# Kernel optimization log

Hardware: AMD Instinct MI355X
Metric: run time of the kernel (lower is better)

## Reference

```python
import jax, jax.numpy as jnp
import numpy as np

N = 50000      # nodes
E = 600000     # edges
F_IN = 128     # num_node_features
H = 128        # hidden_channels
C = 10         # num_classes
G = 128        # graphs in batch


def setup_inputs() -> dict:
    key = jax.random.key(0)
    ks = jax.random.split(key, 12)
    x = jax.random.normal(ks[0], (N, F_IN), dtype=jnp.float32)
    edge_index = jax.random.randint(ks[1], (2, E), 0, N, dtype=jnp.int64)
    batch = jnp.sort(jax.random.randint(ks[2], (N,), 0, G, dtype=jnp.int64))
    s = 0.05
    return {
        "x": x,
        "W1": jax.random.normal(ks[3], (F_IN, H), jnp.float32) * s,
        "b1": jnp.zeros((H,), jnp.float32),
        "W2": jax.random.normal(ks[4], (H, H), jnp.float32) * s,
        "b2": jnp.zeros((H,), jnp.float32),
        "W3": jax.random.normal(ks[5], (H, H), jnp.float32) * s,
        "b3": jnp.zeros((H,), jnp.float32),
        "Wl": jax.random.normal(ks[6], (H, C), jnp.float32) * s,
        "bl": jnp.zeros((C,), jnp.float32),
        "edge_index": edge_index,
        "batch": batch,
    }


def _gcn_conv(h, W, b, src, dst, norm, n):
    # h: [N, din] -> linear (no bias), gather, scale, scatter-add, + bias
    h = h @ W                                  # [N, dout]
    msg = norm[:, None] * h[src]               # [E+N, dout]
    out = jax.ops.segment_sum(msg, dst, num_segments=n)
    return out + b


def reference(x, W1, b1, W2, b2, W3, b3, Wl, bl, edge_index, batch):
    n = x.shape[0]
    # add self-loops (PyG GCNConv default) and symmetric normalization
    loop = jnp.arange(n, dtype=edge_index.dtype)
    src = jnp.concatenate([edge_index[0], loop])   # [E+N]
    dst = jnp.concatenate([edge_index[1], loop])   # [E+N]
    deg = jax.ops.segment_sum(jnp.ones_like(dst, dtype=x.dtype), dst, num_segments=n)
    dinv = jnp.where(deg > 0, jax.lax.rsqrt(deg), 0.0)
    norm = dinv[src] * dinv[dst]                   # [E+N]

    h = jax.nn.relu(_gcn_conv(x, W1, b1, src, dst, norm, n))
    h = jax.nn.relu(_gcn_conv(h, W2, b2, src, dst, norm, n))
    h = jax.nn.relu(_gcn_conv(h, W3, b3, src, dst, norm, n))

    # global mean pool over graph ids
    sums = jax.ops.segment_sum(h, batch, num_segments=G)           # [G, H]
    cnts = jax.ops.segment_sum(jnp.ones((n,), h.dtype), batch, num_segments=G)
    pooled = sums / jnp.maximum(cnts, 1.0)[:, None]

    # dropout is identity at inference; final linear classifier
    return pooled @ Wl + bl                                        # [G, C]
```

## Files before the change

kernel.cpp:

```cpp
#include <hip/hip_runtime.h>

#define HID 128
#define CLS 10
#define RCAP 64

typedef short short8 __attribute__((ext_vector_type(8)));
typedef float f32x4 __attribute__((ext_vector_type(4)));

__device__ __forceinline__ unsigned short f2bf(float f) {
  union { float f; unsigned u; } v; v.f = f;
  unsigned u = v.u;
  return (unsigned short)((u + 0x7FFFu + ((u >> 16) & 1u)) >> 16);
}
__device__ __forceinline__ float bf_lo(unsigned p) { return __uint_as_float(p << 16); }
__device__ __forceinline__ float bf_hi(unsigned p) { return __uint_as_float(p & 0xFFFF0000u); }


__global__ __launch_bounds__(256) void zero_init(int* __restrict__ degi, int n,
                                                 float* __restrict__ pooled, int gh,
                                                 unsigned short* __restrict__ TzA,
                                                 unsigned short* __restrict__ TzB) {
  int i = blockIdx.x * 256 + threadIdx.x;
  if (i < n) degi[i] = 0;
  if (i < gh) pooled[i] = 0.f;
  if (blockIdx.x == 0 && threadIdx.x < 16) {
    uint4 z; z.x = z.y = z.z = z.w = 0u;
    *(uint4*)&TzA[threadIdx.x * 8] = z;
    *(uint4*)&TzB[threadIdx.x * 8] = z;
  }
}

__global__ __launch_bounds__(256) void degree_fill_wt(const int* __restrict__ src,
                                                      const int* __restrict__ dst,
                                                      int* __restrict__ degi,
                                                      int* __restrict__ col_src, int E, int nbE,
                                                      const float* __restrict__ W1,
                                                      const float* __restrict__ W2,
                                                      const float* __restrict__ W3,
                                                      unsigned short* __restrict__ Wt) {
  int b = blockIdx.x;
  if (b < nbE) {
    int e = b * 256 + threadIdx.x;
    if (e >= E) return;
    int d = dst[e];
    int slot = atomicAdd(&degi[d], 1);
    if (slot < RCAP) col_src[(size_t)d * RCAP + slot] = src[e];
    return;
  }
  int wb = b - nbE;
  int mat = wb >> 4;
  int part = wb & 15;
  const float* W = (mat == 0) ? W1 : (mat == 1) ? W2 : W3;
  unsigned short* o = Wt + (size_t)mat * HID * HID;
  int base = part * (HID * HID / 16);
  for (int r = 0; r < HID * HID / 16; r += 256) {
    int idx = base + r + threadIdx.x;
    int k = idx >> 7, nn = idx & 127;
    o[nn * HID + k] = f2bf(W[idx]);
  }
}


#define WTP 136

__global__ __launch_bounds__(256) void gemm_mfma(const float* __restrict__ Aptr,
                                                 const unsigned short* __restrict__ Wt,
                                                 const int* __restrict__ degi,
                                                 unsigned short* __restrict__ Tb,
                                                 int* __restrict__ pad_col,
                                                 int nrows) {
  __shared__ unsigned short sW[HID][WTP];
  int tid = threadIdx.x;
  int wave = tid >> 6, lane = tid & 63;
  int m_lo = lane & 15, quad = lane >> 4;
  int row0 = blockIdx.x * 128;
  int rbase = row0 + wave * 32;

  uint4 araw[2][4];
#pragma unroll
  for (int tr = 0; tr < 2; ++tr) {
    int grow = rbase + tr * 16 + m_lo;
    int gr = (grow < nrows) ? grow : (nrows - 1);
    const float* Arow = Aptr + (size_t)gr * HID;
#pragma unroll
    for (int kb = 0; kb < 4; ++kb) {
      float4 f0 = *(const float4*)&Arow[kb * 32 + quad * 8];
      float4 f1 = *(const float4*)&Arow[kb * 32 + quad * 8 + 4];
      uint4 u;
      u.x = (unsigned)f2bf(f0.x) | ((unsigned)f2bf(f0.y) << 16);
      u.y = (unsigned)f2bf(f0.z) | ((unsigned)f2bf(f0.w) << 16);
      u.z = (unsigned)f2bf(f1.x) | ((unsigned)f2bf(f1.y) << 16);
      u.w = (unsigned)f2bf(f1.z) | ((unsigned)f2bf(f1.w) << 16);
      araw[tr][kb] = u;
    }
  }

  const uint4* Wt4 = (const uint4*)Wt;
#pragma unroll
  for (int i = 0; i < 8; ++i) {
    int idx = i * 256 + tid;
    *(uint4*)&sW[idx >> 4][(idx & 15) * 8] = Wt4[idx];
  }
  __syncthreads();

  f32x4 acc[2][8];
#pragma unroll
  for (int tr = 0; tr < 2; ++tr)
#pragma unroll
    for (int tc = 0; tc < 8; ++tc) acc[tr][tc] = (f32x4)(0.f);

#pragma unroll
  for (int kb = 0; kb < 4; ++kb) {
    short8 b[8];
#pragma unroll
    for (int tc = 0; tc < 8; ++tc) {
      union { uint4 u; short8 s; } cv;
      cv.u = *(const uint4*)&sW[tc * 16 + m_lo][kb * 32 + quad * 8];
      b[tc] = cv.s;
    }
#pragma unroll
    for (int tr = 0; tr < 2; ++tr) {
      union { uint4 u; short8 s; } av;
      av.u = araw[tr][kb];
#pragma unroll
      for (int tc = 0; tc < 8; ++tc)
        acc[tr][tc] = __builtin_amdgcn_mfma_f32_16x16x32_bf16(av.s, b[tc], acc[tr][tc], 0, 0, 0);
    }
  }

#pragma unroll
  for (int tr = 0; tr < 2; ++tr) {
#pragma unroll
    for (int r = 0; r < 4; ++r) {
      int grow = rbase + tr * 16 + quad * 4 + r;
      if (grow < nrows) {
        int dgv = degi[grow];
        float s = rsqrtf((float)dgv + 1.0f);
        unsigned short* orow = &Tb[(size_t)grow * HID];
#pragma unroll
        for (int tc = 0; tc < 8; ++tc)
          orow[tc * 16 + m_lo] = f2bf(s * acc[tr][tc][r]);
        if (m_lo == 0) {
          int d = dgv < RCAP ? dgv : RCAP;
          int dp = (d + 3) & ~3;
          for (int sl = d; sl < dp; ++sl)
            pad_col[(size_t)grow * RCAP + sl] = nrows;
        }
      }
    }
  }
}


__device__ __forceinline__ void agg_node(const unsigned* __restrict__ Tb2,
                                         const int* __restrict__ degi,
                                         const int* __restrict__ col_src,
                                         const float* __restrict__ bias,
                                         int node, int l4, float a[8]) {
  uint4 sv = *(const uint4*)&Tb2[(size_t)node * 64 + l4 * 4];
  a[0] = bf_lo(sv.x); a[1] = bf_hi(sv.x); a[2] = bf_lo(sv.y); a[3] = bf_hi(sv.y);
  a[4] = bf_lo(sv.z); a[5] = bf_hi(sv.z); a[6] = bf_lo(sv.w); a[7] = bf_hi(sv.w);
  int deg = degi[node];
  int dc = deg < RCAP ? deg : RCAP;
  int dp = (dc + 3) & ~3;
  const int* row = &col_src[(size_t)node * RCAP];
  int j = 0;
  for (; j + 8 <= dp; j += 8) {
    int idx[8];
#pragma unroll
    for (int u = 0; u < 8; ++u) idx[u] = row[j + u];
    uint4 v[8];
#pragma unroll
    for (int u = 0; u < 8; ++u) v[u] = *(const uint4*)&Tb2[(size_t)idx[u] * 64 + l4 * 4];
#pragma unroll
    for (int u = 0; u < 8; ++u) {
      a[0] += bf_lo(v[u].x); a[1] += bf_hi(v[u].x);
      a[2] += bf_lo(v[u].y); a[3] += bf_hi(v[u].y);
      a[4] += bf_lo(v[u].z); a[5] += bf_hi(v[u].z);
      a[6] += bf_lo(v[u].w); a[7] += bf_hi(v[u].w);
    }
  }
  if (j < dp) {
    int idx[4];
#pragma unroll
    for (int u = 0; u < 4; ++u) idx[u] = row[j + u];
    uint4 v[4];
#pragma unroll
    for (int u = 0; u < 4; ++u) v[u] = *(const uint4*)&Tb2[(size_t)idx[u] * 64 + l4 * 4];
#pragma unroll
    for (int u = 0; u < 4; ++u) {
      a[0] += bf_lo(v[u].x); a[1] += bf_hi(v[u].x);
      a[2] += bf_lo(v[u].y); a[3] += bf_hi(v[u].y);
      a[4] += bf_lo(v[u].z); a[5] += bf_hi(v[u].z);
      a[6] += bf_lo(v[u].w); a[7] += bf_hi(v[u].w);
    }
  }
  float di = rsqrtf((float)deg + 1.0f);
  float4 bs0 = *(const float4*)&bias[l4 * 8];
  float4 bs1 = *(const float4*)&bias[l4 * 8 + 4];
  a[0] = fmaxf(di * a[0] + bs0.x, 0.f);
  a[1] = fmaxf(di * a[1] + bs0.y, 0.f);
  a[2] = fmaxf(di * a[2] + bs0.z, 0.f);
  a[3] = fmaxf(di * a[3] + bs0.w, 0.f);
  a[4] = fmaxf(di * a[4] + bs1.x, 0.f);
  a[5] = fmaxf(di * a[5] + bs1.y, 0.f);
  a[6] = fmaxf(di * a[6] + bs1.z, 0.f);
  a[7] = fmaxf(di * a[7] + bs1.w, 0.f);
}


__global__ __launch_bounds__(256, 4) void fused_agg_gemm(const unsigned* __restrict__ Tb_in,
                                                         const int* __restrict__ degi,
                                                         const int* __restrict__ col_src,
                                                         const float* __restrict__ bias,
                                                         const unsigned short* __restrict__ Wt,
                                                         unsigned short* __restrict__ Tb_out,
                                                         int n) {
  __shared__ unsigned short sW[HID][WTP];
  __shared__ unsigned short sH[16][WTP];
  int tid = threadIdx.x;

  const uint4* Wt4 = (const uint4*)Wt;
#pragma unroll
  for (int i = 0; i < 8; ++i) {
    int idx = i * 256 + tid;
    *(uint4*)&sW[idx >> 4][(idx & 15) * 8] = Wt4[idx];
  }

  int nl = tid >> 4, l4 = tid & 15;
  int node = blockIdx.x * 16 + nl;
  int nodec = node < n ? node : (n - 1);
  float a[8];
  agg_node(Tb_in, degi, col_src, bias, nodec, l4, a);
  uint4 o;
  o.x = (unsigned)f2bf(a[0]) | ((unsigned)f2bf(a[1]) << 16);
  o.y = (unsigned)f2bf(a[2]) | ((unsigned)f2bf(a[3]) << 16);
  o.z = (unsigned)f2bf(a[4]) | ((unsigned)f2bf(a[5]) << 16);
  o.w = (unsigned)f2bf(a[6]) | ((unsigned)f2bf(a[7]) << 16);
  *(uint4*)&sH[nl][l4 * 8] = o;
  __syncthreads();

  int wid = tid >> 6, lane = tid & 63;
  int m_lo = lane & 15, quad = lane >> 4;
  f32x4 acc[2];
  acc[0] = (f32x4)(0.f); acc[1] = (f32x4)(0.f);
#pragma unroll
  for (int kb = 0; kb < 4; ++kb) {
    union { uint4 u; short8 s; } av;
    av.u = *(const uint4*)&sH[m_lo][kb * 32 + quad * 8];
#pragma unroll
    for (int t = 0; t < 2; ++t) {
      int tc = wid * 2 + t;
      union { uint4 u; short8 s; } bv;
      bv.u = *(const uint4*)&sW[tc * 16 + m_lo][kb * 32 + quad * 8];
      acc[t] = __builtin_amdgcn_mfma_f32_16x16x32_bf16(av.s, bv.s, acc[t], 0, 0, 0);
    }
  }
#pragma unroll
  for (int r = 0; r < 4; ++r) {
    int grow = blockIdx.x * 16 + quad * 4 + r;
    if (grow < n) {
      float s = rsqrtf((float)degi[grow] + 1.0f);
      unsigned short* orow = &Tb_out[(size_t)grow * HID];
#pragma unroll
      for (int t = 0; t < 2; ++t) {
        int tc = wid * 2 + t;
        orow[tc * 16 + m_lo] = f2bf(s * acc[t][r]);
      }
    }
  }
}

#define SPP 132

__global__ __launch_bounds__(256) void aggregate_pool(const unsigned* __restrict__ Tb2,
                                                      const int* __restrict__ degi,
                                                      const int* __restrict__ col_src,
                                                      const float* __restrict__ bias,
                                                      const int* __restrict__ batch,
                                                      float* __restrict__ pooled, int n) {
  __shared__ float sP[16][SPP];
  int tid = threadIdx.x;
  int wave = tid >> 6, lane = tid & 63;
  int sub = lane >> 4;
  int l4 = lane & 15;
  int base = blockIdx.x * 16;
  int nl = wave * 4 + sub;
  int node = base + nl;
  bool active = (node < n);

  float a[8] = {0.f, 0.f, 0.f, 0.f, 0.f, 0.f, 0.f, 0.f};
  if (active) agg_node(Tb2, degi, col_src, bias, node, l4, a);
  *(float4*)&sP[nl][l4 * 8] = make_float4(a[0], a[1], a[2], a[3]);
  *(float4*)&sP[nl][l4 * 8 + 4] = make_float4(a[4], a[5], a[6], a[7]);
  __syncthreads();

  if (tid < HID) {
    int g = -1;
    float acc = 0.f;
    for (int i = 0; i < 16; ++i) {
      int nd = base + i;
      if (nd >= n) break;
      int bi = batch[nd];
      if (bi != g) {
        if (g >= 0) atomicAdd(&pooled[g * HID + tid], acc);
        acc = 0.f;
        g = bi;
      }
      acc += sP[i][tid];
    }
    if (g >= 0) atomicAdd(&pooled[g * HID + tid], acc);
  }
}

__global__ __launch_bounds__(128) void classify_k(const float* __restrict__ pooled,
                                                  const int* __restrict__ batch,
                                                  const float* __restrict__ Wl,
                                                  const float* __restrict__ bl,
                                                  float* __restrict__ out, int n) {
  int g = blockIdx.x;
  int t = threadIdx.x;
  int lo = 0, hi = n;
  while (lo < hi) { int mid = (lo + hi) >> 1; if (batch[mid] < g) lo = mid + 1; else hi = mid; }
  int s = lo;
  hi = n;
  while (lo < hi) { int mid = (lo + hi) >> 1; if (batch[mid] < g + 1) lo = mid + 1; else hi = mid; }
  float c = fmaxf((float)(lo - s), 1.0f);
  __shared__ float p[HID];
  p[t] = pooled[g * HID + t] / c;
  __syncthreads();
  if (t < CLS) {
    float o = bl[t];
    for (int j = 0; j < HID; ++j) o += p[j] * Wl[j * CLS + t];
    out[g * CLS + t] = o;
  }
}


extern "C" void kernel_launch(void* const* d_in, const int* in_sizes, int n_in,
                              void* d_out, int out_size, void* d_ws, size_t ws_size,
                              hipStream_t stream) {
  const float* x  = (const float*)d_in[0];
  const float* W1 = (const float*)d_in[1];
  const float* b1 = (const float*)d_in[2];
  const float* W2 = (const float*)d_in[3];
  const float* b2 = (const float*)d_in[4];
  const float* W3 = (const float*)d_in[5];
  const float* b3 = (const float*)d_in[6];
  const float* Wl = (const float*)d_in[7];
  const float* bl = (const float*)d_in[8];
  const int* edge_index = (const int*)d_in[9];
  const int* batch = (const int*)d_in[10];

  const int N = in_sizes[10];
  const int E = in_sizes[9] / 2;
  const int G = out_size / CLS;
  const int* src = edge_index;
  const int* dst = edge_index + E;

  uintptr_t p = (uintptr_t)d_ws;
  auto take = [&](size_t bytes) -> void* {
    void* r = (void*)p;
    p += (bytes + 255) & ~(size_t)255;
    return r;
  };
  int*      degi      = (int*)take((size_t)N * 4);
  int*      col_src   = (int*)take((size_t)N * RCAP * 4);
  unsigned short* WtA = (unsigned short*)take((size_t)3 * HID * HID * 2);
  unsigned short* bufTa = (unsigned short*)take((size_t)(N + 1) * HID * 2);
  unsigned short* bufTb = (unsigned short*)take((size_t)(N + 1) * HID * 2);
  float*    pooled    = (float*)take((size_t)G * HID * 4);

  int nbN = (N + 255) / 256;
  int nbE = (E + 255) / 256;

  zero_init<<<nbN, 256, 0, stream>>>(degi, N, pooled, G * HID,
                                     bufTa + (size_t)N * HID, bufTb + (size_t)N * HID);
  degree_fill_wt<<<nbE + 48, 256, 0, stream>>>(src, dst, degi, col_src, E, nbE,
                                               W1, W2, W3, WtA);

  int gemmBlocks = (N + 127) / 128;
  int aggBlocks = (N + 15) / 16;

  gemm_mfma<<<gemmBlocks, 256, 0, stream>>>(x, WtA, degi, bufTa, col_src, N);
  fused_agg_gemm<<<aggBlocks, 256, 0, stream>>>((unsigned*)bufTa, degi, col_src, b1,
                                                WtA + (size_t)HID * HID, bufTb, N);
  fused_agg_gemm<<<aggBlocks, 256, 0, stream>>>((unsigned*)bufTb, degi, col_src, b2,
                                                WtA + (size_t)2 * HID * HID, bufTa, N);
  aggregate_pool<<<aggBlocks, 256, 0, stream>>>((unsigned*)bufTa, degi, col_src, b3,
                                                batch, pooled, N);
  classify_k<<<G, 128, 0, stream>>>(pooled, batch, Wl, bl, (float*)d_out, N);
}
```

Measured before the change: 226.0 us.

## Split feature matrix into column slices and aggregate one slice per launch

Stores the bf16 node-feature buffers as four 32-column slices, each of 64 bytes per node, instead of 128-column rows. Each aggregation pass then gathers from a single slice across several launches, so the gathered working set is smaller and more likely to stay in cache. Four lanes cooperate on each neighbor list and combine their partial sums with shuffles. The fused aggregate+GEMM kernel now aggregates only the last slice and reads the other three from an intermediate buffer. This adds extra launches, an extra buffer round trip and repeated index-list reads.

```diff
diff --git a/kernel.cpp b/kernel.cpp
--- a/kernel.cpp
+++ b/kernel.cpp
@@ -6,6 +6,7 @@
 
 typedef short short8 __attribute__((ext_vector_type(8)));
 typedef float f32x4 __attribute__((ext_vector_type(4)));
+
 
 __device__ __forceinline__ unsigned short f2bf(float f) {
   union { float f; unsigned u; } v; v.f = f;
@@ -18,15 +19,18 @@
 
 __global__ __launch_bounds__(256) void zero_init(int* __restrict__ degi, int n,
                                                  float* __restrict__ pooled, int gh,
-                                                 unsigned short* __restrict__ TzA,
-                                                 unsigned short* __restrict__ TzB) {
+                                                 unsigned short* __restrict__ Ta,
+                                                 unsigned short* __restrict__ Tb) {
   int i = blockIdx.x * 256 + threadIdx.x;
   if (i < n) degi[i] = 0;
   if (i < gh) pooled[i] = 0.f;
-  if (blockIdx.x == 0 && threadIdx.x < 16) {
+  if (blockIdx.x == 0 && threadIdx.x < 32) {
+    int buf = threadIdx.x >> 4;
+    int s = (threadIdx.x >> 2) & 3;
+    int c = threadIdx.x & 3;
+    unsigned short* T = buf ? Tb : Ta;
     uint4 z; z.x = z.y = z.z = z.w = 0u;
-    *(uint4*)&TzA[threadIdx.x * 8] = z;
-    *(uint4*)&TzB[threadIdx.x * 8] = z;
+    *(uint4*)&T[((size_t)s * (n + 1) + n) * 32 + c * 8] = z;
   }
 }
 
@@ -136,10 +140,10 @@
       if (grow < nrows) {
         int dgv = degi[grow];
         float s = rsqrtf((float)dgv + 1.0f);
-        unsigned short* orow = &Tb[(size_t)grow * HID];
 #pragma unroll
         for (int tc = 0; tc < 8; ++tc)
-          orow[tc * 16 + m_lo] = f2bf(s * acc[tr][tc][r]);
+          Tb[((size_t)(tc >> 1) * (nrows + 1) + grow) * 32 + (tc & 1) * 16 + m_lo] =
+              f2bf(s * acc[tr][tc][r]);
         if (m_lo == 0) {
           int d = dgv < RCAP ? dgv : RCAP;
           int dp = (d + 3) & ~3;
@@ -152,69 +156,84 @@
 }
 
 
-__device__ __forceinline__ void agg_node(const unsigned* __restrict__ Tb2,
-                                         const int* __restrict__ degi,
-                                         const int* __restrict__ col_src,
-                                         const float* __restrict__ bias,
-                                         int node, int l4, float a[8]) {
-  uint4 sv = *(const uint4*)&Tb2[(size_t)node * 64 + l4 * 4];
-  a[0] = bf_lo(sv.x); a[1] = bf_hi(sv.x); a[2] = bf_lo(sv.y); a[3] = bf_hi(sv.y);
-  a[4] = bf_lo(sv.z); a[5] = bf_hi(sv.z); a[6] = bf_lo(sv.w); a[7] = bf_hi(sv.w);
-  int deg = degi[node];
-  int dc = deg < RCAP ? deg : RCAP;
-  int dp = (dc + 3) & ~3;
-  const int* row = &col_src[(size_t)node * RCAP];
-  int j = 0;
-  for (; j + 8 <= dp; j += 8) {
-    int idx[8];
-#pragma unroll
-    for (int u = 0; u < 8; ++u) idx[u] = row[j + u];
-    uint4 v[8];
-#pragma unroll
-    for (int u = 0; u < 8; ++u) v[u] = *(const uint4*)&Tb2[(size_t)idx[u] * 64 + l4 * 4];
-#pragma unroll
-    for (int u = 0; u < 8; ++u) {
-      a[0] += bf_lo(v[u].x); a[1] += bf_hi(v[u].x);
-      a[2] += bf_lo(v[u].y); a[3] += bf_hi(v[u].y);
-      a[4] += bf_lo(v[u].z); a[5] += bf_hi(v[u].z);
-      a[6] += bf_lo(v[u].w); a[7] += bf_hi(v[u].w);
-    }
+__device__ __forceinline__ void slice_gather(const unsigned short* __restrict__ Tslice,
+                                             const int* __restrict__ row,
+                                             int node, int dp, int q, int sub, float a[8]) {
+  if (q == 0) {
+    uint4 sv = *(const uint4*)&Tslice[(size_t)node * 32 + sub * 8];
+    a[0] = bf_lo(sv.x); a[1] = bf_hi(sv.x); a[2] = bf_lo(sv.y); a[3] = bf_hi(sv.y);
+    a[4] = bf_lo(sv.z); a[5] = bf_hi(sv.z); a[6] = bf_lo(sv.w); a[7] = bf_hi(sv.w);
+  } else {
+#pragma unroll
+    for (int k = 0; k < 8; ++k) a[k] = 0.f;
+  }
+  int j = q;
+  for (; j + 4 < dp; j += 8) {
+    int i0 = row[j], i1 = row[j + 4];
+    uint4 v0 = *(const uint4*)&Tslice[(size_t)i0 * 32 + sub * 8];
+    uint4 v1 = *(const uint4*)&Tslice[(size_t)i1 * 32 + sub * 8];
+    a[0] += bf_lo(v0.x); a[1] += bf_hi(v0.x); a[2] += bf_lo(v0.y); a[3] += bf_hi(v0.y);
+    a[4] += bf_lo(v0.z); a[5] += bf_hi(v0.z); a[6] += bf_lo(v0.w); a[7] += bf_hi(v0.w);
+    a[0] += bf_lo(v1.x); a[1] += bf_hi(v1.x); a[2] += bf_lo(v1.y); a[3] += bf_hi(v1.y);
+    a[4] += bf_lo(v1.z); a[5] += bf_hi(v1.z); a[6] += bf_lo(v1.w); a[7] += bf_hi(v1.w);
   }
   if (j < dp) {
-    int idx[4];
-#pragma unroll
-    for (int u = 0; u < 4; ++u) idx[u] = row[j + u];
-    uint4 v[4];
-#pragma unroll
-    for (int u = 0; u < 4; ++u) v[u] = *(const uint4*)&Tb2[(size_t)idx[u] * 64 + l4 * 4];
-#pragma unroll
-    for (int u = 0; u < 4; ++u) {
-      a[0] += bf_lo(v[u].x); a[1] += bf_hi(v[u].x);
-      a[2] += bf_lo(v[u].y); a[3] += bf_hi(v[u].y);
-      a[4] += bf_lo(v[u].z); a[5] += bf_hi(v[u].z);
-      a[6] += bf_lo(v[u].w); a[7] += bf_hi(v[u].w);
-    }
-  }
-  float di = rsqrtf((float)deg + 1.0f);
-  float4 bs0 = *(const float4*)&bias[l4 * 8];
-  float4 bs1 = *(const float4*)&bias[l4 * 8 + 4];
-  a[0] = fmaxf(di * a[0] + bs0.x, 0.f);
-  a[1] = fmaxf(di * a[1] + bs0.y, 0.f);
-  a[2] = fmaxf(di * a[2] + bs0.z, 0.f);
-  a[3] = fmaxf(di * a[3] + bs0.w, 0.f);
-  a[4] = fmaxf(di * a[4] + bs1.x, 0.f);
-  a[5] = fmaxf(di * a[5] + bs1.y, 0.f);
-  a[6] = fmaxf(di * a[6] + bs1.z, 0.f);
-  a[7] = fmaxf(di * a[7] + bs1.w, 0.f);
-}
-
-
-__global__ __launch_bounds__(256, 4) void fused_agg_gemm(const unsigned* __restrict__ Tb_in,
+    int i0 = row[j];
+    uint4 v0 = *(const uint4*)&Tslice[(size_t)i0 * 32 + sub * 8];
+    a[0] += bf_lo(v0.x); a[1] += bf_hi(v0.x); a[2] += bf_lo(v0.y); a[3] += bf_hi(v0.y);
+    a[4] += bf_lo(v0.z); a[5] += bf_hi(v0.z); a[6] += bf_lo(v0.w); a[7] += bf_hi(v0.w);
+  }
+#pragma unroll
+  for (int k = 0; k < 8; ++k) {
+    a[k] += __shfl_xor(a[k], 4, 64);
+    a[k] += __shfl_xor(a[k], 8, 64);
+  }
+}
+
+__global__ __launch_bounds__(256) void agg_slice(const unsigned short* __restrict__ Tin,
+                                                 const int* __restrict__ degi,
+                                                 const int* __restrict__ col_src,
+                                                 const float* __restrict__ bias,
+                                                 unsigned short* __restrict__ Hout,
+                                                 int n, int s) {
+  int tid = threadIdx.x;
+  int g = tid >> 4, l4 = tid & 15;
+  int q = l4 >> 2, sub = l4 & 3;
+  const unsigned short* Tslice = Tin + (size_t)s * (n + 1) * 32;
+  float4 b0 = *(const float4*)&bias[s * 32 + sub * 8];
+  float4 b1 = *(const float4*)&bias[s * 32 + sub * 8 + 4];
+  for (int c = 0; c < 2; ++c) {
+    int node = blockIdx.x * 32 + g * 2 + c;
+    if (node >= n) return;
+    int deg = degi[node];
+    int dc = deg < RCAP ? deg : RCAP;
+    int dp = (dc + 3) & ~3;
+    const int* row = &col_src[(size_t)node * RCAP];
+    float a[8];
+    slice_gather(Tslice, row, node, dp, q, sub, a);
+    float di = rsqrtf((float)deg + 1.0f);
+    a[0] = fmaxf(di * a[0] + b0.x, 0.f); a[1] = fmaxf(di * a[1] + b0.y, 0.f);
+    a[2] = fmaxf(di * a[2] + b0.z, 0.f); a[3] = fmaxf(di * a[3] + b0.w, 0.f);
+    a[4] = fmaxf(di * a[4] + b1.x, 0.f); a[5] = fmaxf(di * a[5] + b1.y, 0.f);
+    a[6] = fmaxf(di * a[6] + b1.z, 0.f); a[7] = fmaxf(di * a[7] + b1.w, 0.f);
+    if (q == 0) {
+      uint4 o;
+      o.x = (unsigned)f2bf(a[0]) | ((unsigned)f2bf(a[1]) << 16);
+      o.y = (unsigned)f2bf(a[2]) | ((unsigned)f2bf(a[3]) << 16);
+      o.z = (unsigned)f2bf(a[4]) | ((unsigned)f2bf(a[5]) << 16);
+      o.w = (unsigned)f2bf(a[6]) | ((unsigned)f2bf(a[7]) << 16);
+      *(uint4*)&Hout[((size_t)s * (n + 1) + node) * 32 + sub * 8] = o;
+    }
+  }
+}
+
+__global__ __launch_bounds__(256, 4) void agg_slice_gemm(const unsigned short* __restrict__ Tin,
                                                          const int* __restrict__ degi,
                                                          const int* __restrict__ col_src,
                                                          const float* __restrict__ bias,
+                                                         const unsigned short* __restrict__ Hs,
                                                          const unsigned short* __restrict__ Wt,
-                                                         unsigned short* __restrict__ Tb_out,
+                                                         unsigned short* __restrict__ Tout,
                                                          int n) {
   __shared__ unsigned short sW[HID][WTP];
   __shared__ unsigned short sH[16][WTP];
@@ -227,17 +246,44 @@
     *(uint4*)&sW[idx >> 4][(idx & 15) * 8] = Wt4[idx];
   }
 
-  int nl = tid >> 4, l4 = tid & 15;
-  int node = blockIdx.x * 16 + nl;
+  if (tid < 192) {
+    int node_l = tid / 12;
+    int r = tid % 12;
+    int s2 = r >> 2, c = r & 3;
+    int gnode = blockIdx.x * 16 + node_l;
+    if (gnode >= n) gnode = n - 1;
+    uint4 v = *(const uint4*)&Hs[((size_t)s2 * (n + 1) + gnode) * 32 + c * 8];
+    *(uint4*)&sH[node_l][s2 * 32 + c * 8] = v;
+  }
+
+  int g = tid >> 4, l4 = tid & 15;
+  int q = l4 >> 2, sub = l4 & 3;
+  int node = blockIdx.x * 16 + g;
   int nodec = node < n ? node : (n - 1);
-  float a[8];
-  agg_node(Tb_in, degi, col_src, bias, nodec, l4, a);
-  uint4 o;
-  o.x = (unsigned)f2bf(a[0]) | ((unsigned)f2bf(a[1]) << 16);
-  o.y = (unsigned)f2bf(a[2]) | ((unsigned)f2bf(a[3]) << 16);
-  o.z = (unsigned)f2bf(a[4]) | ((unsigned)f2bf(a[5]) << 16);
-  o.w = (unsigned)f2bf(a[6]) | ((unsigned)f2bf(a[7]) << 16);
-  *(uint4*)&sH[nl][l4 * 8] = o;
+  const unsigned short* Tslice = Tin + (size_t)3 * (n + 1) * 32;
+  {
+    int deg = degi[nodec];
+    int dc = deg < RCAP ? deg : RCAP;
+    int dp = (dc + 3) & ~3;
+    const int* row = &col_src[(size_t)nodec * RCAP];
+    float a[8];
+    slice_gather(Tslice, row, nodec, dp, q, sub, a);
+    float di = rsqrtf((float)deg + 1.0f);
+    float4 b0 = *(const float4*)&bias[96 + sub * 8];
+    float4 b1 = *(const float4*)&bias[96 + sub * 8 + 4];
+    a[0] = fmaxf(di * a[0] + b0.x, 0.f); a[1] = fmaxf(di * a[1] + b0.y, 0.f);
+    a[2] = fmaxf(di * a[2] + b0.z, 0.f); a[3] = fmaxf(di * a[3] + b0.w, 0.f);
+    a[4] = fmaxf(di * a[4] + b1.x, 0.f); a[5] = fmaxf(di * a[5] + b1.y, 0.f);
+    a[6] = fmaxf(di * a[6] + b1.z, 0.f); a[7] = fmaxf(di * a[7] + b1.w, 0.f);
+    if (q == 0) {
+      uint4 o;
+      o.x = (unsigned)f2bf(a[0]) | ((unsigned)f2bf(a[1]) << 16);
+      o.y = (unsigned)f2bf(a[2]) | ((unsigned)f2bf(a[3]) << 16);
+      o.z = (unsigned)f2bf(a[4]) | ((unsigned)f2bf(a[5]) << 16);
+      o.w = (unsigned)f2bf(a[6]) | ((unsigned)f2bf(a[7]) << 16);
+      *(uint4*)&sH[g][96 + sub * 8] = o;
+    }
+  }
   __syncthreads();
 
   int wid = tid >> 6, lane = tid & 63;
@@ -261,55 +307,66 @@
     int grow = blockIdx.x * 16 + quad * 4 + r;
     if (grow < n) {
       float s = rsqrtf((float)degi[grow] + 1.0f);
-      unsigned short* orow = &Tb_out[(size_t)grow * HID];
 #pragma unroll
       for (int t = 0; t < 2; ++t) {
         int tc = wid * 2 + t;
-        orow[tc * 16 + m_lo] = f2bf(s * acc[t][r]);
+        Tout[((size_t)(tc >> 1) * (n + 1) + grow) * 32 + (tc & 1) * 16 + m_lo] =
+            f2bf(s * acc[t][r]);
       }
     }
   }
 }
 
-#define SPP 132
-
-__global__ __launch_bounds__(256) void aggregate_pool(const unsigned* __restrict__ Tb2,
-                                                      const int* __restrict__ degi,
-                                                      const int* __restrict__ col_src,
-                                                      const float* __restrict__ bias,
-                                                      const int* __restrict__ batch,
-                                                      float* __restrict__ pooled, int n) {
-  __shared__ float sP[16][SPP];
+__global__ __launch_bounds__(256) void pool_slice(const unsigned short* __restrict__ Tin,
+                                                  const int* __restrict__ degi,
+                                                  const int* __restrict__ col_src,
+                                                  const float* __restrict__ bias,
+                                                  const int* __restrict__ batch,
+                                                  float* __restrict__ pooled, int n, int s) {
+  __shared__ float sP[16][36];
   int tid = threadIdx.x;
-  int wave = tid >> 6, lane = tid & 63;
-  int sub = lane >> 4;
-  int l4 = lane & 15;
+  int g = tid >> 4, l4 = tid & 15;
+  int q = l4 >> 2, sub = l4 & 3;
   int base = blockIdx.x * 16;
-  int nl = wave * 4 + sub;
-  int node = base + nl;
-  bool active = (node < n);
-
-  float a[8] = {0.f, 0.f, 0.f, 0.f, 0.f, 0.f, 0.f, 0.f};
-  if (active) agg_node(Tb2, degi, col_src, bias, node, l4, a);
-  *(float4*)&sP[nl][l4 * 8] = make_float4(a[0], a[1], a[2], a[3]);
-  *(float4*)&sP[nl][l4 * 8 + 4] = make_float4(a[4], a[5], a[6], a[7]);
+  int node = base + g;
+  const unsigned short* Tslice = Tin + (size_t)s * (n + 1) * 32;
+  if (node < n) {
+    int deg = degi[node];
+    int dc = deg < RCAP ? deg : RCAP;
+    int dp = (dc + 3) & ~3;
+    const int* row = &col_src[(size_t)node * RCAP];
+    float a[8];
+    slice_gather(Tslice, row, node, dp, q, sub, a);
+    float di = rsqrtf((float)deg + 1.0f);
+    float4 b0 = *(const float4*)&bias[s * 32 + sub * 8];
+    float4 b1 = *(const float4*)&bias[s * 32 + sub * 8 + 4];
+    a[0] = fmaxf(di * a[0] + b0.x, 0.f); a[1] = fmaxf(di * a[1] + b0.y, 0.f);
+    a[2] = fmaxf(di * a[2] + b0.z, 0.f); a[3] = fmaxf(di * a[3] + b0.w, 0.f);
+    a[4] = fmaxf(di * a[4] + b1.x, 0.f); a[5] = fmaxf(di * a[5] + b1.y, 0.f);
+    a[6] = fmaxf(di * a[6] + b1.z, 0.f); a[7] = fmaxf(di * a[7] + b1.w, 0.f);
+    if (q == 0) {
+      *(float4*)&sP[g][sub * 8] = make_float4(a[0], a[1], a[2], a[3]);
+      *(float4*)&sP[g][sub * 8 + 4] = make_float4(a[4], a[5], a[6], a[7]);
+    }
+  }
   __syncthreads();
 
-  if (tid < HID) {
-    int g = -1;
+  if (tid < 32) {
+    int f = tid;
+    int gq = -1;
     float acc = 0.f;
     for (int i = 0; i < 16; ++i) {
       int nd = base + i;
       if (nd >= n) break;
       int bi = batch[nd];
-      if (bi != g) {
-        if (g >= 0) atomicAdd(&pooled[g * HID + tid], acc);
+      if (bi != gq) {
+        if (gq >= 0) atomicAdd(&pooled[gq * HID + s * 32 + f], acc);
         acc = 0.f;
-        g = bi;
+        gq = bi;
       }
-      acc += sP[i][tid];
-    }
-    if (g >= 0) atomicAdd(&pooled[g * HID + tid], acc);
+      acc += sP[i][f];
+    }
+    if (gq >= 0) atomicAdd(&pooled[gq * HID + s * 32 + f], acc);
   }
 }
 
@@ -369,25 +426,34 @@
   unsigned short* WtA = (unsigned short*)take((size_t)3 * HID * HID * 2);
   unsigned short* bufTa = (unsigned short*)take((size_t)(N + 1) * HID * 2);
   unsigned short* bufTb = (unsigned short*)take((size_t)(N + 1) * HID * 2);
+  unsigned short* bufH  = (unsigned short*)take((size_t)(N + 1) * HID * 2);
   float*    pooled    = (float*)take((size_t)G * HID * 4);
 
   int nbN = (N + 255) / 256;
   int nbE = (E + 255) / 256;
 
-  zero_init<<<nbN, 256, 0, stream>>>(degi, N, pooled, G * HID,
-                                     bufTa + (size_t)N * HID, bufTb + (size_t)N * HID);
+  zero_init<<<nbN, 256, 0, stream>>>(degi, N, pooled, G * HID, bufTa, bufTb);
   degree_fill_wt<<<nbE + 48, 256, 0, stream>>>(src, dst, degi, col_src, E, nbE,
                                                W1, W2, W3, WtA);
 
   int gemmBlocks = (N + 127) / 128;
+  int sliceBlocks = (N + 31) / 32;
   int aggBlocks = (N + 15) / 16;
 
   gemm_mfma<<<gemmBlocks, 256, 0, stream>>>(x, WtA, degi, bufTa, col_src, N);
-  fused_agg_gemm<<<aggBlocks, 256, 0, stream>>>((unsigned*)bufTa, degi, col_src, b1,
+
+  for (int s = 0; s < 3; ++s)
+    agg_slice<<<sliceBlocks, 256, 0, stream>>>(bufTa, degi, col_src, b1, bufH, N, s);
+  agg_slice_gemm<<<aggBlocks, 256, 0, stream>>>(bufTa, degi, col_src, b1, bufH,
                                                 WtA + (size_t)HID * HID, bufTb, N);
-  fused_agg_gemm<<<aggBlocks, 256, 0, stream>>>((unsigned*)bufTb, degi, col_src, b2,
+
+  for (int s = 0; s < 3; ++s)
+    agg_slice<<<sliceBlocks, 256, 0, stream>>>(bufTb, degi, col_src, b2, bufH, N, s);
+  agg_slice_gemm<<<aggBlocks, 256, 0, stream>>>(bufTb, degi, col_src, b2, bufH,
                                                 WtA + (size_t)2 * HID * HID, bufTa, N);
-  aggregate_pool<<<aggBlocks, 256, 0, stream>>>((unsigned*)bufTa, degi, col_src, b3,
-                                                batch, pooled, N);
+
+  for (int s = 0; s < 4; ++s)
+    pool_slice<<<aggBlocks, 256, 0, stream>>>(bufTa, degi, col_src, b3, batch, pooled, N, s);
+
   classify_k<<<G, 128, 0, stream>>>(pooled, batch, Wl, bl, (float*)d_out, N);
 }
```

After: 300.2 us. +32.8%, slower.
